# Performance work log

Measured on AMD Instinct MI355X. Metric: run time of the kernel, lower is better.

Reference implementation:

```python
import jax, jax.numpy as jnp
import numpy as np


def setup_inputs() -> dict:
    key = jax.random.key(0)
    ks = jax.random.split(key, 10)
    B, S, C, H, NC, T = 128, 512, 512, 512, 64, 25
    s = 0.02  # init scale
    return {
        "x": jax.random.normal(ks[0], (B, S, C), jnp.float32),
        "text": jax.random.randint(ks[1], (B, T + 1), 0, NC),
        "W_i2h": jax.random.normal(ks[2], (C, H), jnp.float32) * s,
        "W_h2h": jax.random.normal(ks[3], (H, H), jnp.float32) * s,
        "b_h2h": jnp.zeros((H,), jnp.float32),
        "W_score": jax.random.normal(ks[4], (H, 1), jnp.float32) * s,
        "W_lstm": jax.random.normal(ks[5], (C + NC, 4 * H), jnp.float32) * s,
        "U_lstm": jax.random.normal(ks[6], (H, 4 * H), jnp.float32) * s,
        "b_lstm": jnp.zeros((4 * H,), jnp.float32),
        "W_gen": jax.random.normal(ks[7], (H, NC), jnp.float32) * s,
        "b_gen": jnp.zeros((NC,), jnp.float32),
        "batch_max_length": 25,
    }


def reference(x, text, W_i2h, W_h2h, b_h2h, W_score, W_lstm, U_lstm, b_lstm,
              W_gen, b_gen, batch_max_length):
    B = x.shape[0]
    H = W_h2h.shape[0]
    NC = W_gen.shape[1]
    T = batch_max_length

    # i2h(batch_H) is loop-invariant -> compute once. [B,S,H]
    batch_H_proj = jnp.einsum('bsc,ch->bsh', x, W_i2h)
    # one-hot teacher-forcing inputs, time-major for scan. [T,B,NC]
    onehots_t = jnp.swapaxes(jax.nn.one_hot(text[:, :T], NC, dtype=x.dtype), 0, 1)

    def step(carry, char_oh):
        h, c = carry
        hp = (h @ W_h2h + b_h2h)[:, None, :]                 # [B,1,H]
        e = jnp.tanh(batch_H_proj + hp) @ W_score            # [B,S,1]
        alpha = jax.nn.softmax(e, axis=1)                    # [B,S,1]
        context = jnp.einsum('bs,bsc->bc', alpha[..., 0], x) # [B,C]
        inp = jnp.concatenate([context, char_oh], axis=1)    # [B,C+NC]
        # Keras LSTMCell gate math: z split into i,f,g,o chunks
        z = inp @ W_lstm + h @ U_lstm + b_lstm               # [B,4H]
        zi, zf, zg, zo = jnp.split(z, 4, axis=1)
        i = jax.nn.sigmoid(zi)
        f = jax.nn.sigmoid(zf)
        g = jnp.tanh(zg)
        o = jax.nn.sigmoid(zo)
        c_new = f * c + i * g
        h_new = o * jnp.tanh(c_new)
        return (h_new, c_new), h_new

    init = (jnp.zeros((B, H), x.dtype), jnp.zeros((B, H), x.dtype))
    _, hs = jax.lax.scan(step, init, onehots_t)              # [T,B,H]
    output_hiddens = jnp.swapaxes(hs, 0, 1)                  # [B,T,H]
    probs = output_hiddens @ W_gen + b_gen                   # [B,T,NC]
    return probs
```

## Files before the change

kernel.cpp:

```cpp
#include <hip/hip_runtime.h>
#include <hip/hip_bf16.h>

#define B_ 128
#define S_ 512
#define C_ 512
#define H_ 512
#define NC_ 64
#define T_ 25
#define TEXTW (T_ + 1)

typedef __attribute__((ext_vector_type(8))) short bf16x8;
typedef __attribute__((ext_vector_type(8))) unsigned short u16x8;
typedef __attribute__((ext_vector_type(4))) float f32x4;

__device__ __forceinline__ float bf2f(unsigned short u) {
    union { unsigned int i; float f; } v; v.i = ((unsigned int)u) << 16; return v.f;
}
__device__ __forceinline__ unsigned short f2bf(float f) {
    union { float f; unsigned int u; } v; v.f = f;
    unsigned int r = (v.u + 0x7FFFu + ((v.u >> 16) & 1u)) >> 16;
    return (unsigned short)r;
}
__device__ __forceinline__ void gload_lds16(const void* g, void* l) {
    __builtin_amdgcn_global_load_lds(
        (const __attribute__((address_space(1))) unsigned int*)g,
        (__attribute__((address_space(3))) unsigned int*)l, 16, 0, 0);
}
__device__ __forceinline__ float fast_tanh(float x) {
    float e = __builtin_amdgcn_exp2f(2.885390082f * x);
    return 1.f - 2.f * __builtin_amdgcn_rcpf(e + 1.f);
}
__device__ __forceinline__ float fast_sigmoid(float x) {
    return __builtin_amdgcn_rcpf(1.f + __builtin_amdgcn_exp2f(-1.442695041f * x));
}

__global__ __launch_bounds__(512) void setup_k(
    const float* __restrict__ Wi, const float* __restrict__ Wh,
    const float* __restrict__ Wl, const float* __restrict__ Ul,
    unsigned short* __restrict__ Wt_bf, unsigned short* __restrict__ Wh_bf,
    unsigned short* __restrict__ WU_t,
    float* __restrict__ c2, unsigned short* __restrict__ inp) {
    int blk = blockIdx.x, tid = threadIdx.x;
    if (blk < 128) {
        c2[blk * 512 + tid] = 0.f;
        c2[65536 + blk * 512 + tid] = 0.f;
        inp[blk * 1024 + 512 + tid] = 0;
    } else if (blk < 640) {
        int n = blk - 128;
        Wt_bf[n * 512 + tid] = f2bf(Wi[tid * 512 + n]);
    } else if (blk < 1152) {
        int i = (blk - 640) * 512 + tid;
        Wh_bf[i] = f2bf(Wh[i]);
    } else {
        int np = blk - 1152;
        int h = np >> 2, g = np & 3;
        {
            float v = Wl[(size_t)tid * 2048 + g * 512 + h];
            WU_t[(size_t)np * 1024 + tid] = f2bf(v);
        }
        {
            float v = Ul[(size_t)tid * 2048 + g * 512 + h];
            WU_t[(size_t)np * 1024 + 512 + tid] = f2bf(v);
        }
    }
}

__global__ __launch_bounds__(256) void conv_x(const float* __restrict__ in,
                                              unsigned short* __restrict__ out) {
    int i = blockIdx.x * 256 + threadIdx.x;
    const float4 v = ((const float4*)in)[i];
    ushort4 o;
    o.x = f2bf(v.x); o.y = f2bf(v.y); o.z = f2bf(v.z); o.w = f2bf(v.w);
    ((ushort4*)out)[i] = o;
}

__global__ __launch_bounds__(512) void gemm_proj(const unsigned short* __restrict__ A,
                                                 const unsigned short* __restrict__ Bt,
                                                 unsigned short* __restrict__ Cm) {
    __shared__ unsigned short As[256 * 64];
    __shared__ unsigned short Bs[128 * 64];
    int tid = threadIdx.x;
    int lane = tid & 63;
    int wid = tid >> 6;
    int wr = wid >> 1, wc = wid & 1;
    int row0 = blockIdx.y * 256;
    int col0 = blockIdx.x * 128;

    f32x4 acc[4][4];
#pragma unroll
    for (int i = 0; i < 4; ++i)
#pragma unroll
        for (int j = 0; j < 4; ++j) acc[i][j] = (f32x4){0.f, 0.f, 0.f, 0.f};

    for (int k0 = 0; k0 < 512; k0 += 64) {
#pragma unroll
        for (int i = 0; i < 4; ++i) {
            int e = tid + i * 512;
            int r = e >> 3, cc = e & 7;
            int cs = cc ^ (r & 7);
            gload_lds16(A + (size_t)(row0 + r) * 512 + k0 + cs * 8, &As[e * 8]);
        }
#pragma unroll
        for (int i = 0; i < 2; ++i) {
            int e = tid + i * 512;
            int r = e >> 3, cc = e & 7;
            int cs = cc ^ (r & 7);
            gload_lds16(Bt + (size_t)(col0 + r) * 512 + k0 + cs * 8, &Bs[e * 8]);
        }
        __syncthreads();
#pragma unroll
        for (int ks = 0; ks < 2; ++ks) {
            bf16x8 a[4], b[4];
#pragma unroll
            for (int i = 0; i < 4; ++i) {
                int m = wr * 64 + i * 16 + (lane & 15);
                int ch = (ks * 4 + (lane >> 4)) ^ (m & 7);
                a[i] = *(const bf16x8*)&As[(m * 8 + ch) * 8];
            }
#pragma unroll
            for (int j = 0; j < 4; ++j) {
                int n = wc * 64 + j * 16 + (lane & 15);
                int ch = (ks * 4 + (lane >> 4)) ^ (n & 7);
                b[j] = *(const bf16x8*)&Bs[(n * 8 + ch) * 8];
            }
#pragma unroll
            for (int i = 0; i < 4; ++i)
#pragma unroll
                for (int j = 0; j < 4; ++j)
                    acc[i][j] = __builtin_amdgcn_mfma_f32_16x16x32_bf16(a[i], b[j], acc[i][j], 0, 0, 0);
        }
        __syncthreads();
    }
#pragma unroll
    for (int i = 0; i < 4; ++i)
#pragma unroll
        for (int j = 0; j < 4; ++j) {
            int gcol = col0 + wc * 64 + j * 16 + (lane & 15);
#pragma unroll
            for (int r = 0; r < 4; ++r) {
                int grow = row0 + wr * 64 + i * 16 + (lane >> 4) * 4 + r;
                Cm[(size_t)grow * 512 + gcol] = f2bf(acc[i][j][r]);
            }
        }
}

__global__ __launch_bounds__(512) void z_gemm(
    const unsigned short* __restrict__ inp, const unsigned short* __restrict__ Bt,
    const float* __restrict__ pc, const float* __restrict__ pm,
    const float* __restrict__ ps, float* __restrict__ Z) {
    __shared__ unsigned short As[128 * 128];
    __shared__ unsigned short Bs[32 * 128];
    int tid = threadIdx.x;
    int lane = tid & 63;
    int wave = tid >> 6;
    int wr = wave >> 1, wc = wave & 1;
    int col0 = blockIdx.x * 32;

    float cw0[4], cw1[4];
    int rr[4], csv[4];
#pragma unroll
    for (int i = 0; i < 4; ++i) {
        int e = tid + i * 512;
        int r = e >> 4, cc = e & 15;
        rr[i] = r; csv[i] = cc ^ (r & 15);
        float m0 = pm[r], m1 = pm[128 + r];
        float s0 = ps[r], s1 = ps[128 + r];
        float M = fmaxf(m0, m1);
        float w0 = __builtin_amdgcn_exp2f(1.442695041f * (m0 - M));
        float w1 = __builtin_amdgcn_exp2f(1.442695041f * (m1 - M));
        float inv = 1.f / (w0 * s0 + w1 * s1);
        cw0[i] = w0 * inv; cw1[i] = w1 * inv;
    }

    f32x4 acc[2];
#pragma unroll
    for (int i = 0; i < 2; ++i) acc[i] = (f32x4){0.f, 0.f, 0.f, 0.f};

    for (int k0 = 0; k0 < 1024; k0 += 128) {
        if (k0 < 512) {
#pragma unroll
            for (int i = 0; i < 4; ++i) {
                int e = tid + i * 512;
                int kb = k0 + csv[i] * 8;
                const float* c0p = pc + rr[i] * 512 + kb;
                const float* c1p = pc + 65536 + rr[i] * 512 + kb;
                float4 c0a = *(const float4*)c0p;
                float4 c0b = *(const float4*)(c0p + 4);
                float4 c1a = *(const float4*)c1p;
                float4 c1b = *(const float4*)(c1p + 4);
                u16x8 o;
                o[0] = f2bf(cw0[i] * c0a.x + cw1[i] * c1a.x);
                o[1] = f2bf(cw0[i] * c0a.y + cw1[i] * c1a.y);
                o[2] = f2bf(cw0[i] * c0a.z + cw1[i] * c1a.z);
                o[3] = f2bf(cw0[i] * c0a.w + cw1[i] * c1a.w);
                o[4] = f2bf(cw0[i] * c0b.x + cw1[i] * c1b.x);
                o[5] = f2bf(cw0[i] * c0b.y + cw1[i] * c1b.y);
                o[6] = f2bf(cw0[i] * c0b.z + cw1[i] * c1b.z);
                o[7] = f2bf(cw0[i] * c0b.w + cw1[i] * c1b.w);
                *(u16x8*)&As[e * 8] = o;
            }
        } else {
#pragma unroll
            for (int i = 0; i < 4; ++i) {
                int e = tid + i * 512;
                gload_lds16(inp + (size_t)rr[i] * 1024 + k0 + csv[i] * 8, &As[e * 8]);
            }
        }
        {
            int e = tid;
            int r = e >> 4, cc = e & 15;
            int cs = cc ^ (r & 15);
            gload_lds16(Bt + (size_t)(col0 + r) * 1024 + k0 + cs * 8, &Bs[e * 8]);
        }
        __syncthreads();
#pragma unroll
        for (int ks = 0; ks < 4; ++ks) {
            bf16x8 a[2], bfr;
#pragma unroll
            for (int i = 0; i < 2; ++i) {
                int m = wr * 32 + i * 16 + (lane & 15);
                int ch = (ks * 4 + (lane >> 4)) ^ (m & 15);
                a[i] = *(const bf16x8*)&As[(m * 16 + ch) * 8];
            }
            {
                int n = wc * 16 + (lane & 15);
                int ch = (ks * 4 + (lane >> 4)) ^ (n & 15);
                bfr = *(const bf16x8*)&Bs[(n * 16 + ch) * 8];
            }
#pragma unroll
            for (int i = 0; i < 2; ++i)
                acc[i] = __builtin_amdgcn_mfma_f32_16x16x32_bf16(a[i], bfr, acc[i], 0, 0, 0);
        }
        __syncthreads();
    }
#pragma unroll
    for (int i = 0; i < 2; ++i) {
        int gcol = col0 + wc * 16 + (lane & 15);
#pragma unroll
        for (int r = 0; r < 4; ++r) {
            int grow = wr * 32 + i * 16 + (lane >> 4) * 4 + r;
            Z[(size_t)grow * 2048 + gcol] = acc[i][r];
        }
    }
}

__global__ __launch_bounds__(1024) void ghp_e2(
    const float* __restrict__ z, const int* __restrict__ text,
    const float* __restrict__ Wl, const float* __restrict__ bl,
    const unsigned short* __restrict__ Whb, const float* __restrict__ bh2h,
    float* __restrict__ c2, float* __restrict__ hs_t,
    unsigned short* __restrict__ inp,
    const unsigned short* __restrict__ proj, const unsigned short* __restrict__ xb,
    const float* __restrict__ Wscore,
    float* __restrict__ pc, float* __restrict__ pm, float* __restrict__ ps, int t) {
    __shared__ float shg[512];
    __shared__ float gp[16][512];
    __shared__ float sh_hp[512];
    __shared__ float sh_e[256];
    __shared__ float sh_alpha[256];
    __shared__ float sh_red[8];
    __shared__ float shp[8][512];
    int blk = blockIdx.x;
    int half = blk >> 7, b = blk & 127;
    int tid = threadIdx.x, wave = tid >> 6, lane = tid & 63;

    if (t >= 0) {
        if (tid < 512) {
            int ch = text[b * TEXTW + t];
            const float* wrow = Wl + (size_t)(512 + ch) * 2048;
            float4 zv = *(const float4*)(z + (size_t)b * 2048 + tid * 4);
            float zi = zv.x + bl[tid] + wrow[tid];
            float zf = zv.y + bl[512 + tid] + wrow[512 + tid];
            float zg = zv.z + bl[1024 + tid] + wrow[1024 + tid];
            float zo = zv.w + bl[1536 + tid] + wrow[1536 + tid];
            float ig = fast_sigmoid(zi);
            float fg = fast_sigmoid(zf);
            float gg = fast_tanh(zg);
            float og = fast_sigmoid(zo);
            int idx = half * 65536 + b * 512 + tid;
            float cn = fg * c2[idx] + ig * gg;
            c2[idx] = cn;
            float hn = og * fast_tanh(cn);
            if (half == 0) {
                hs_t[b * 512 + tid] = hn;
                inp[b * 1024 + 512 + tid] = f2bf(hn);
            }
            shg[tid] = hn;
        }
        __syncthreads();
        if (t >= T_ - 1) return;
        {
            float r8[8] = {0.f, 0.f, 0.f, 0.f, 0.f, 0.f, 0.f, 0.f};
#pragma unroll 4
            for (int kk = 0; kk < 32; ++kk) {
                int k = wave * 32 + kk;
                float hv = shg[k];
                u16x8 wv = *(const u16x8*)(Whb + k * 512 + lane * 8);
#pragma unroll
                for (int jj = 0; jj < 8; ++jj) r8[jj] = fmaf(hv, bf2f(wv[jj]), r8[jj]);
            }
#pragma unroll
            for (int jj = 0; jj < 8; ++jj) gp[wave][lane * 8 + jj] = r8[jj];
        }
        __syncthreads();
        if (tid < 512) {
            float s = bh2h[tid];
#pragma unroll
            for (int w = 0; w < 16; ++w) s += gp[w][tid];
            sh_hp[tid] = s;
        }
        __syncthreads();
    } else {
        if (tid < 512) sh_hp[tid] = bh2h[tid];
        __syncthreads();
    }

    {
        float4 h0 = *(const float4*)(sh_hp + lane * 8);
        float4 h1 = *(const float4*)(sh_hp + lane * 8 + 4);
        float4 w0 = *(const float4*)(Wscore + lane * 8);
        float4 w1 = *(const float4*)(Wscore + lane * 8 + 4);
        float hp_r[8] = {h0.x, h0.y, h0.z, h0.w, h1.x, h1.y, h1.z, h1.w};
        float w_r[8]  = {w0.x, w0.y, w0.z, w0.w, w1.x, w1.y, w1.z, w1.w};
        float w2_r[8];
#pragma unroll
        for (int j = 0; j < 8; ++j) w2_r[j] = -2.f * w_r[j];
        int s0g = half * 256 + wave * 16;
        for (int i = 0; i < 16; i += 4) {
            bf16x8 pv[4];
#pragma unroll
            for (int q = 0; q < 4; ++q)
                pv[q] = *(const bf16x8*)(proj + ((size_t)(b * 512 + s0g + i + q) << 9) + lane * 8);
#pragma unroll
            for (int q = 0; q < 4; ++q) {
                float a = 0.f;
#pragma unroll
                for (int j = 0; j < 8; ++j) {
                    float xv = bf2f((unsigned short)pv[q][j]) + hp_r[j];
                    float r = __builtin_amdgcn_rcpf(__builtin_amdgcn_exp2f(2.885390082f * xv) + 1.f);
                    a += w_r[j];
                    a = fmaf(w2_r[j], r, a);
                }
#pragma unroll
                for (int off = 32; off > 0; off >>= 1) a += __shfl_xor(a, off, 64);
                if (lane == 0) sh_e[wave * 16 + i + q] = a;
            }
        }
    }
    __syncthreads();

    if (tid < 256) {
        float v = sh_e[tid];
        float m = v;
#pragma unroll
        for (int off = 32; off > 0; off >>= 1) m = fmaxf(m, __shfl_xor(m, off, 64));
        if (lane == 0) sh_red[wave] = m;
    }
    __syncthreads();
    if (tid < 256) {
        float mh = fmaxf(fmaxf(sh_red[0], sh_red[1]), fmaxf(sh_red[2], sh_red[3]));
        float p = __builtin_amdgcn_exp2f(1.442695041f * (sh_e[tid] - mh));
        float ss = p;
#pragma unroll
        for (int off = 32; off > 0; off >>= 1) ss += __shfl_xor(ss, off, 64);
        if (lane == 0) sh_red[4 + wave] = ss;
        sh_alpha[tid] = p;
    }
    __syncthreads();
    if (tid == 0) {
        pm[half * 128 + b] = fmaxf(fmaxf(sh_red[0], sh_red[1]), fmaxf(sh_red[2], sh_red[3]));
        ps[half * 128 + b] = sh_red[4] + sh_red[5] + sh_red[6] + sh_red[7];
    }

    {
        int cc = wave >> 3, sg = wave & 7;
        int col = cc * 256 + lane * 4;
        float a0 = 0.f, a1 = 0.f, a2 = 0.f, a3 = 0.f;
#pragma unroll 4
        for (int sl = sg; sl < 256; sl += 8) {
            float al = sh_alpha[sl];
            int s = half * 256 + sl;
            ushort4 xv = *(const ushort4*)(xb + ((size_t)(b * 512 + s) << 9) + col);
            a0 = fmaf(al, bf2f(xv.x), a0);
            a1 = fmaf(al, bf2f(xv.y), a1);
            a2 = fmaf(al, bf2f(xv.z), a2);
            a3 = fmaf(al, bf2f(xv.w), a3);
        }
        *(float4*)&shp[sg][col] = make_float4(a0, a1, a2, a3);
    }
    __syncthreads();
    if (tid < 512) {
        float s = 0.f;
#pragma unroll
        for (int r = 0; r < 8; ++r) s += shp[r][tid];
        pc[(size_t)(half * 128 + b) * 512 + tid] = s;
    }
}

__global__ __launch_bounds__(64) void gen_probs(const float* __restrict__ hs,
                                                const float* __restrict__ Wg,
                                                const float* __restrict__ bg,
                                                float* __restrict__ out) {
    __shared__ float sh[8][512];
    int r0 = blockIdx.x * 8;
    int tid = threadIdx.x;
#pragma unroll
    for (int q = 0; q < 8; ++q) {
        int row = r0 + q;
        int b = row / T_, t = row % T_;
        const float* hrow = hs + ((size_t)t * B_ + b) * H_;
        for (int i = tid; i < 512; i += 64) sh[q][i] = hrow[i];
    }
    __syncthreads();
    float acc[8];
#pragma unroll
    for (int q = 0; q < 8; ++q) acc[q] = bg[tid];
#pragma unroll 4
    for (int k = 0; k < 512; ++k) {
        float w = Wg[k * 64 + tid];
#pragma unroll
        for (int q = 0; q < 8; ++q) acc[q] = fmaf(sh[q][k], w, acc[q]);
    }
#pragma unroll
    for (int q = 0; q < 8; ++q) out[(size_t)(r0 + q) * 64 + tid] = acc[q];
}

extern "C" void kernel_launch(void* const* d_in, const int* in_sizes, int n_in,
                              void* d_out, int out_size, void* d_ws, size_t ws_size,
                              hipStream_t stream) {
    const float* x       = (const float*)d_in[0];
    const int*   text    = (const int*)d_in[1];
    const float* W_i2h   = (const float*)d_in[2];
    const float* W_h2h   = (const float*)d_in[3];
    const float* b_h2h   = (const float*)d_in[4];
    const float* W_score = (const float*)d_in[5];
    const float* W_lstm  = (const float*)d_in[6];
    const float* U_lstm  = (const float*)d_in[7];
    const float* b_lstm  = (const float*)d_in[8];
    const float* W_gen   = (const float*)d_in[9];
    const float* b_gen   = (const float*)d_in[10];
    float* out = (float*)d_out;

    char* ws = (char*)d_ws;
    unsigned short* x_bf    = (unsigned short*)ws;
    unsigned short* proj_bf = (unsigned short*)(ws + 67108864);
    unsigned short* Wt_bf   = (unsigned short*)(ws + 134217728);
    unsigned short* Wh_bf   = (unsigned short*)(ws + 134742016);
    unsigned short* WU_t    = (unsigned short*)(ws + 135266304);
    float* c2      = (float*)(ws + 139460608);
    unsigned short* inp_bf = (unsigned short*)(ws + 139984896);
    float* z_buf   = (float*)(ws + 140247040);
    float* pc      = (float*)(ws + 141295616);
    float* pm      = (float*)(ws + 141819904);
    float* ps      = (float*)(ws + 141820928);
    float* hs      = (float*)(ws + 141821952);

    setup_k<<<dim3(3200), 512, 0, stream>>>(W_i2h, W_h2h, W_lstm, U_lstm,
                                            Wt_bf, Wh_bf, WU_t, c2, inp_bf);
    conv_x<<<dim3(32768), 256, 0, stream>>>(x, x_bf);
    gemm_proj<<<dim3(4, 256), 512, 0, stream>>>(x_bf, Wt_bf, proj_bf);
    ghp_e2<<<dim3(256), 1024, 0, stream>>>(z_buf, text, W_lstm, b_lstm, Wh_bf, b_h2h,
                                           c2, hs, inp_bf, proj_bf, x_bf, W_score,
                                           pc, pm, ps, -1);
    for (int t = 0; t < T_; ++t) {
        z_gemm<<<dim3(64), 512, 0, stream>>>(inp_bf, WU_t, pc, pm, ps, z_buf);
        ghp_e2<<<dim3(256), 1024, 0, stream>>>(z_buf, text, W_lstm, b_lstm, Wh_bf, b_h2h,
                                               c2, hs + (size_t)t * (B_ * H_),
                                               inp_bf, proj_bf, x_bf, W_score,
                                               pc, pm, ps, t);
    }
    gen_probs<<<dim3(400), 64, 0, stream>>>(hs, W_gen, b_gen, out);
}
```

Baseline: 1.343 ms.

## Fold x bf16 conversion into setup kernel and widen projection GEMM tile

Merges the standalone x fp32-to-bf16 conversion kernel into the setup kernel as extra blocks, removing one launch. The projection GEMM tile grows from 256x128 to 256x256 per block, so each wave now computes 128x64 and the A tile is reused across more columns. The trade-off is more accumulator registers per wave (32 f32x4) and only 512 blocks, which may lower occupancy.

```diff
diff --git a/kernel.cpp b/kernel.cpp
--- a/kernel.cpp
+++ b/kernel.cpp
@@ -35,24 +35,34 @@
 }
 
 __global__ __launch_bounds__(512) void setup_k(
-    const float* __restrict__ Wi, const float* __restrict__ Wh,
-    const float* __restrict__ Wl, const float* __restrict__ Ul,
-    unsigned short* __restrict__ Wt_bf, unsigned short* __restrict__ Wh_bf,
-    unsigned short* __restrict__ WU_t,
+    const float* __restrict__ x, const float* __restrict__ Wi,
+    const float* __restrict__ Wh, const float* __restrict__ Wl,
+    const float* __restrict__ Ul,
+    unsigned short* __restrict__ x_bf, unsigned short* __restrict__ Wt_bf,
+    unsigned short* __restrict__ Wh_bf, unsigned short* __restrict__ WU_t,
     float* __restrict__ c2, unsigned short* __restrict__ inp) {
     int blk = blockIdx.x, tid = threadIdx.x;
-    if (blk < 128) {
-        c2[blk * 512 + tid] = 0.f;
-        c2[65536 + blk * 512 + tid] = 0.f;
-        inp[blk * 1024 + 512 + tid] = 0;
-    } else if (blk < 640) {
-        int n = blk - 128;
+    if (blk < 16384) {
+        int i = blk * 512 + tid;
+        const float4 v = ((const float4*)x)[i];
+        ushort4 o;
+        o.x = f2bf(v.x); o.y = f2bf(v.y); o.z = f2bf(v.z); o.w = f2bf(v.w);
+        ((ushort4*)x_bf)[i] = o;
+        return;
+    }
+    int b2 = blk - 16384;
+    if (b2 < 128) {
+        c2[b2 * 512 + tid] = 0.f;
+        c2[65536 + b2 * 512 + tid] = 0.f;
+        inp[b2 * 1024 + 512 + tid] = 0;
+    } else if (b2 < 640) {
+        int n = b2 - 128;
         Wt_bf[n * 512 + tid] = f2bf(Wi[tid * 512 + n]);
-    } else if (blk < 1152) {
-        int i = (blk - 640) * 512 + tid;
+    } else if (b2 < 1152) {
+        int i = (b2 - 640) * 512 + tid;
         Wh_bf[i] = f2bf(Wh[i]);
     } else {
-        int np = blk - 1152;
+        int np = b2 - 1152;
         int h = np >> 2, g = np & 3;
         {
             float v = Wl[(size_t)tid * 2048 + g * 512 + h];
@@ -65,30 +75,21 @@
     }
 }
 
-__global__ __launch_bounds__(256) void conv_x(const float* __restrict__ in,
-                                              unsigned short* __restrict__ out) {
-    int i = blockIdx.x * 256 + threadIdx.x;
-    const float4 v = ((const float4*)in)[i];
-    ushort4 o;
-    o.x = f2bf(v.x); o.y = f2bf(v.y); o.z = f2bf(v.z); o.w = f2bf(v.w);
-    ((ushort4*)out)[i] = o;
-}
-
 __global__ __launch_bounds__(512) void gemm_proj(const unsigned short* __restrict__ A,
                                                  const unsigned short* __restrict__ Bt,
                                                  unsigned short* __restrict__ Cm) {
     __shared__ unsigned short As[256 * 64];
-    __shared__ unsigned short Bs[128 * 64];
+    __shared__ unsigned short Bs[256 * 64];
     int tid = threadIdx.x;
     int lane = tid & 63;
     int wid = tid >> 6;
-    int wr = wid >> 1, wc = wid & 1;
+    int wr = wid >> 2, wc = wid & 3;
     int row0 = blockIdx.y * 256;
-    int col0 = blockIdx.x * 128;
-
-    f32x4 acc[4][4];
-#pragma unroll
-    for (int i = 0; i < 4; ++i)
+    int col0 = blockIdx.x * 256;
+
+    f32x4 acc[8][4];
+#pragma unroll
+    for (int i = 0; i < 8; ++i)
 #pragma unroll
         for (int j = 0; j < 4; ++j) acc[i][j] = (f32x4){0.f, 0.f, 0.f, 0.f};
 
@@ -101,7 +102,7 @@
             gload_lds16(A + (size_t)(row0 + r) * 512 + k0 + cs * 8, &As[e * 8]);
         }
 #pragma unroll
-        for (int i = 0; i < 2; ++i) {
+        for (int i = 0; i < 4; ++i) {
             int e = tid + i * 512;
             int r = e >> 3, cc = e & 7;
             int cs = cc ^ (r & 7);
@@ -110,10 +111,10 @@
         __syncthreads();
 #pragma unroll
         for (int ks = 0; ks < 2; ++ks) {
-            bf16x8 a[4], b[4];
-#pragma unroll
-            for (int i = 0; i < 4; ++i) {
-                int m = wr * 64 + i * 16 + (lane & 15);
+            bf16x8 a[8], b[4];
+#pragma unroll
+            for (int i = 0; i < 8; ++i) {
+                int m = wr * 128 + i * 16 + (lane & 15);
                 int ch = (ks * 4 + (lane >> 4)) ^ (m & 7);
                 a[i] = *(const bf16x8*)&As[(m * 8 + ch) * 8];
             }
@@ -124,7 +125,7 @@
                 b[j] = *(const bf16x8*)&Bs[(n * 8 + ch) * 8];
             }
 #pragma unroll
-            for (int i = 0; i < 4; ++i)
+            for (int i = 0; i < 8; ++i)
 #pragma unroll
                 for (int j = 0; j < 4; ++j)
                     acc[i][j] = __builtin_amdgcn_mfma_f32_16x16x32_bf16(a[i], b[j], acc[i][j], 0, 0, 0);
@@ -132,13 +133,13 @@
         __syncthreads();
     }
 #pragma unroll
-    for (int i = 0; i < 4; ++i)
+    for (int i = 0; i < 8; ++i)
 #pragma unroll
         for (int j = 0; j < 4; ++j) {
             int gcol = col0 + wc * 64 + j * 16 + (lane & 15);
 #pragma unroll
             for (int r = 0; r < 4; ++r) {
-                int grow = row0 + wr * 64 + i * 16 + (lane >> 4) * 4 + r;
+                int grow = row0 + wr * 128 + i * 16 + (lane >> 4) * 4 + r;
                 Cm[(size_t)grow * 512 + gcol] = f2bf(acc[i][j][r]);
             }
         }
@@ -455,10 +456,9 @@
     float* ps      = (float*)(ws + 141820928);
     float* hs      = (float*)(ws + 141821952);
 
-    setup_k<<<dim3(3200), 512, 0, stream>>>(W_i2h, W_h2h, W_lstm, U_lstm,
-                                            Wt_bf, Wh_bf, WU_t, c2, inp_bf);
-    conv_x<<<dim3(32768), 256, 0, stream>>>(x, x_bf);
-    gemm_proj<<<dim3(4, 256), 512, 0, stream>>>(x_bf, Wt_bf, proj_bf);
+    setup_k<<<dim3(19584), 512, 0, stream>>>(x, W_i2h, W_h2h, W_lstm, U_lstm,
+                                             x_bf, Wt_bf, Wh_bf, WU_t, c2, inp_bf);
+    gemm_proj<<<dim3(2, 256), 512, 0, stream>>>(x_bf, Wt_bf, proj_bf);
     ghp_e2<<<dim3(256), 1024, 0, stream>>>(z_buf, text, W_lstm, b_lstm, Wh_bf, b_h2h,
                                            c2, hs, inp_bf, proj_bf, x_bf, W_score,
                                            pc, pm, ps, -1);
```

After: 1.358 ms. About the same (+1.1%).
